# Performance work log

Measured on AMD Instinct MI355X. Metric: run time of the kernel, lower is better.

## Reference

```python
import jax, jax.numpy as jnp
import numpy as np

N, E, F_IN, H, C = 10000, 640000, 128, 128, 40


def setup_inputs() -> dict:
    key = jax.random.key(0)
    ks = jax.random.split(key, 8)
    x = jax.random.normal(ks[0], (N, F_IN), dtype=jnp.float32)
    edge_index = jax.random.randint(ks[1], (2, E), 0, N, dtype=jnp.int64)
    W1 = jax.random.normal(ks[2], (F_IN, H), dtype=jnp.float32) / np.sqrt(F_IN)
    b1 = jnp.zeros((H,), dtype=jnp.float32)
    W2 = jax.random.normal(ks[3], (H, H), dtype=jnp.float32) / np.sqrt(H)
    b2 = jnp.zeros((H,), dtype=jnp.float32)
    Wc = jax.random.normal(ks[4], (H, C), dtype=jnp.float32) / np.sqrt(H)
    bc = jnp.zeros((C,), dtype=jnp.float32)
    return {"x": x, "edge_index": edge_index, "W1": W1, "b1": b1,
            "W2": W2, "b2": b2, "Wc": Wc, "bc": bc}


def _gcn_conv(x, src, dst, norm, W, b):
    # GCNConv: out = D^{-1/2}(A+I)D^{-1/2} (x @ W) + b
    h = x @ W                               # [N, H]
    msg = h[src] * norm[:, None]            # gather + per-edge normalize
    out = jax.ops.segment_sum(msg, dst, num_segments=N)  # scatter-add
    return out + b


def reference(x, edge_index, W1, b1, W2, b2, Wc, bc):
    # add self-loops (as PyG GCNConv does by default)
    loops = jnp.arange(N, dtype=edge_index.dtype)
    src = jnp.concatenate([edge_index[0], loops])   # [E+N]
    dst = jnp.concatenate([edge_index[1], loops])   # [E+N]
    # symmetric normalization deg^{-1/2} with self-loops included
    deg = jax.ops.segment_sum(jnp.ones_like(dst, dtype=x.dtype), dst, num_segments=N)
    dinv = jax.lax.rsqrt(deg)                       # deg >= 1 due to self-loops
    norm = dinv[src] * dinv[dst]                    # [E+N]

    h = _gcn_conv(x, src, dst, norm, W1, b1)
    h = jax.nn.relu(h)
    h = _gcn_conv(h, src, dst, norm, W2, b2)
    logits = h @ Wc + bc                            # [N, C]
    return jax.nn.log_softmax(logits, axis=1)
```

## Files before the change

kernel.cpp:

```cpp
#include <hip/hip_runtime.h>
#include <hip/hip_fp16.h>
#include <math.h>

#define FDIM 128
#define CDIM 40
#define DMAX 192
#define NMAX 10240
#define SLICE_SHIFT 14
#define SLICE_SZ (1 << SLICE_SHIFT)

__device__ __forceinline__ uint2 pack_half4(float4 v) {
    __half2 p0 = __float22half2_rn(make_float2(v.x, v.y));
    __half2 p1 = __float22half2_rn(make_float2(v.z, v.w));
    uint2 u;
    u.x = *(unsigned int*)&p0;
    u.y = *(unsigned int*)&p1;
    return u;
}

__device__ __forceinline__ void unpack_add4(float acc[8], uint4 r) {
    __half2* p = (__half2*)&r;
    #pragma unroll
    for (int q = 0; q < 4; ++q) {
        float2 f = __half22float2(p[q]);
        acc[2 * q]     += f.x;
        acc[2 * q + 1] += f.y;
    }
}

__global__ __launch_bounds__(256) void k_hist(
        const int* __restrict__ dst, unsigned short* __restrict__ lrank,
        int* __restrict__ cnt, int e, int n) {
    __shared__ int h[NMAX];
    int tid = threadIdx.x;
    for (int i = tid; i < n; i += 256) h[i] = 0;
    __syncthreads();
    int base = (int)blockIdx.x << SLICE_SHIFT;
    int end = base + SLICE_SZ; if (end > e) end = e;
    for (int i = base + tid * 4; i < end; i += 1024) {
        if (i + 3 < end) {
            int4 d = *(const int4*)(dst + i);
            int p0 = atomicAdd(&h[d.x], 1);
            int p1 = atomicAdd(&h[d.y], 1);
            int p2 = atomicAdd(&h[d.z], 1);
            int p3 = atomicAdd(&h[d.w], 1);
            ushort4 r;
            r.x = (unsigned short)p0; r.y = (unsigned short)p1;
            r.z = (unsigned short)p2; r.w = (unsigned short)p3;
            *(ushort4*)(lrank + i) = r;
        } else {
            for (int k = i; k < end; ++k)
                lrank[k] = (unsigned short)atomicAdd(&h[dst[k]], 1);
        }
    }
    __syncthreads();
    int* c = cnt + (size_t)blockIdx.x * n;
    for (int i = tid; i < n; i += 256) c[i] = h[i];
}

__global__ __launch_bounds__(256) void k_scan(
        int* __restrict__ cnt, int* __restrict__ deg, int nslice, int n) {
    int v = blockIdx.x * 256 + threadIdx.x;
    if (v >= n) return;
    int s = 0;
    for (int b = 0; b < nslice; ++b) {
        int t = cnt[(size_t)b * n + v];
        cnt[(size_t)b * n + v] = s;
        s += t;
    }
    deg[v] = s;
}

__global__ __launch_bounds__(256) void k_mega(
        const float* __restrict__ A, const float* __restrict__ W,
        const int* __restrict__ deg, uint2* __restrict__ h16, int n,
        const int* __restrict__ src, const int* __restrict__ dst,
        const unsigned short* __restrict__ lrank, const int* __restrict__ base,
        unsigned short* __restrict__ col, int e, int gemm_blocks) {
    __shared__ float As[32][FDIM];
    int tid = threadIdx.x;
    if ((int)blockIdx.x < gemm_blocks) {
        int r0 = blockIdx.x * 32;
        for (int t = tid; t < 32 * 32; t += 256) {
            int r = t >> 5, c4 = t & 31;
            int gr = r0 + r;
            float4 v = make_float4(0.f, 0.f, 0.f, 0.f);
            if (gr < n) v = ((const float4*)A)[(size_t)gr * 32 + c4];
            ((float4*)As[r])[c4] = v;
        }
        __syncthreads();
        int cb = (tid & 31) * 4;
        int rb = (tid >> 5) * 4;
        float4 acc0 = make_float4(0,0,0,0), acc1 = acc0, acc2 = acc0, acc3 = acc0;
        for (int k = 0; k < FDIM; ++k) {
            float4 w = *(const float4*)(W + k * FDIM + cb);
            float a0 = As[rb + 0][k], a1 = As[rb + 1][k];
            float a2 = As[rb + 2][k], a3 = As[rb + 3][k];
            acc0.x += a0 * w.x; acc0.y += a0 * w.y; acc0.z += a0 * w.z; acc0.w += a0 * w.w;
            acc1.x += a1 * w.x; acc1.y += a1 * w.y; acc1.z += a1 * w.z; acc1.w += a1 * w.w;
            acc2.x += a2 * w.x; acc2.y += a2 * w.y; acc2.z += a2 * w.z; acc2.w += a2 * w.w;
            acc3.x += a3 * w.x; acc3.y += a3 * w.y; acc3.z += a3 * w.z; acc3.w += a3 * w.w;
        }
        float4 accs[4] = {acc0, acc1, acc2, acc3};
        #pragma unroll
        for (int i = 0; i < 4; ++i) {
            int gr = r0 + rb + i;
            if (gr < n) {
                float dinv = rsqrtf((float)(deg[gr] + 1));
                float4 v = accs[i];
                v.x *= dinv; v.y *= dinv; v.z *= dinv; v.w *= dinv;
                h16[(size_t)gr * 32 + (cb >> 2)] = pack_half4(v);
            }
        }
    } else {
        int g = ((int)blockIdx.x - gemm_blocks) * 256 + tid;
        int i4 = g * 4;
        if (i4 + 3 < e) {
            const int* bs = base + (size_t)(i4 >> SLICE_SHIFT) * n;
            int4 d = ((const int4*)dst)[g];
            int4 s = ((const int4*)src)[g];
            ushort4 lr = ((const ushort4*)lrank)[g];
            int p0 = bs[d.x] + lr.x;
            int p1 = bs[d.y] + lr.y;
            int p2 = bs[d.z] + lr.z;
            int p3 = bs[d.w] + lr.w;
            if (p0 < DMAX) col[(size_t)d.x * DMAX + p0] = (unsigned short)s.x;
            if (p1 < DMAX) col[(size_t)d.y * DMAX + p1] = (unsigned short)s.y;
            if (p2 < DMAX) col[(size_t)d.z * DMAX + p2] = (unsigned short)s.z;
            if (p3 < DMAX) col[(size_t)d.w * DMAX + p3] = (unsigned short)s.w;
        } else if (i4 < e) {
            for (int k = i4; k < e; ++k) {
                int d = dst[k];
                int p = base[(size_t)(k >> SLICE_SHIFT) * n + d] + lrank[k];
                if (p < DMAX) col[(size_t)d * DMAX + p] = (unsigned short)src[k];
            }
        }
    }
}

template <bool RELU>
__device__ __forceinline__ void agg_gather(
        float out8[8], const uint4* __restrict__ hs,
        const unsigned short* __restrict__ col, const int* __restrict__ deg,
        const float* __restrict__ bias, int node, int l) {
    int dn = deg[node];
    float dinv = rsqrtf((float)(dn + 1));
    if (dn > DMAX) dn = DMAX;
    const uint4* cl8 = (const uint4*)(col + (size_t)node * DMAX);
    float a0[8], a1[8];
    #pragma unroll
    for (int q = 0; q < 8; ++q) { a0[q] = 0.f; a1[q] = 0.f; }
    unpack_add4(a0, hs[(size_t)node * 16 + l]);
    int j = 0;
    for (; j + 16 <= dn; j += 16) {
        uint4 cA = cl8[(j >> 3) + 0];
        uint4 cB = cl8[(j >> 3) + 1];
        int s0 = cA.x & 0xFFFF, s1 = cA.x >> 16;
        int s2 = cA.y & 0xFFFF, s3 = cA.y >> 16;
        int s4 = cA.z & 0xFFFF, s5 = cA.z >> 16;
        int s6 = cA.w & 0xFFFF, s7 = cA.w >> 16;
        int s8 = cB.x & 0xFFFF, s9 = cB.x >> 16;
        int sa = cB.y & 0xFFFF, sb = cB.y >> 16;
        int sc = cB.z & 0xFFFF, sd = cB.z >> 16;
        int se = cB.w & 0xFFFF, sf = cB.w >> 16;
        uint4 q0 = hs[(size_t)s0 * 16 + l];
        uint4 q1 = hs[(size_t)s1 * 16 + l];
        uint4 q2 = hs[(size_t)s2 * 16 + l];
        uint4 q3 = hs[(size_t)s3 * 16 + l];
        uint4 q4 = hs[(size_t)s4 * 16 + l];
        uint4 q5 = hs[(size_t)s5 * 16 + l];
        uint4 q6 = hs[(size_t)s6 * 16 + l];
        uint4 q7 = hs[(size_t)s7 * 16 + l];
        uint4 q8 = hs[(size_t)s8 * 16 + l];
        uint4 q9 = hs[(size_t)s9 * 16 + l];
        uint4 qa = hs[(size_t)sa * 16 + l];
        uint4 qb = hs[(size_t)sb * 16 + l];
        uint4 qc = hs[(size_t)sc * 16 + l];
        uint4 qd = hs[(size_t)sd * 16 + l];
        uint4 qe = hs[(size_t)se * 16 + l];
        uint4 qf = hs[(size_t)sf * 16 + l];
        unpack_add4(a0, q0); unpack_add4(a1, q1);
        unpack_add4(a0, q2); unpack_add4(a1, q3);
        unpack_add4(a0, q4); unpack_add4(a1, q5);
        unpack_add4(a0, q6); unpack_add4(a1, q7);
        unpack_add4(a0, q8); unpack_add4(a1, q9);
        unpack_add4(a0, qa); unpack_add4(a1, qb);
        unpack_add4(a0, qc); unpack_add4(a1, qd);
        unpack_add4(a0, qe); unpack_add4(a1, qf);
    }
    for (; j + 8 <= dn; j += 8) {
        uint4 c = cl8[j >> 3];
        int s0 = c.x & 0xFFFF, s1 = c.x >> 16;
        int s2 = c.y & 0xFFFF, s3 = c.y >> 16;
        int s4 = c.z & 0xFFFF, s5 = c.z >> 16;
        int s6 = c.w & 0xFFFF, s7 = c.w >> 16;
        uint4 q0 = hs[(size_t)s0 * 16 + l];
        uint4 q1 = hs[(size_t)s1 * 16 + l];
        uint4 q2 = hs[(size_t)s2 * 16 + l];
        uint4 q3 = hs[(size_t)s3 * 16 + l];
        uint4 q4 = hs[(size_t)s4 * 16 + l];
        uint4 q5 = hs[(size_t)s5 * 16 + l];
        uint4 q6 = hs[(size_t)s6 * 16 + l];
        uint4 q7 = hs[(size_t)s7 * 16 + l];
        unpack_add4(a0, q0); unpack_add4(a1, q1);
        unpack_add4(a0, q2); unpack_add4(a1, q3);
        unpack_add4(a0, q4); unpack_add4(a1, q5);
        unpack_add4(a0, q6); unpack_add4(a1, q7);
    }
    const unsigned short* cl = col + (size_t)node * DMAX;
    for (; j < dn; ++j) unpack_add4(a0, hs[(size_t)cl[j] * 16 + l]);
    float4 b0 = ((const float4*)bias)[2 * l];
    float4 b1 = ((const float4*)bias)[2 * l + 1];
    float bb[8] = {b0.x, b0.y, b0.z, b0.w, b1.x, b1.y, b1.z, b1.w};
    #pragma unroll
    for (int q = 0; q < 8; ++q) {
        float v = dinv * (a0[q] + a1[q]) + bb[q];
        out8[q] = RELU ? fmaxf(v, 0.f) : v;
    }
}

__global__ __launch_bounds__(128) void k_agg_gemm(
        const uint4* __restrict__ hs1, const unsigned short* __restrict__ col,
        const int* __restrict__ deg, const float* __restrict__ b1,
        const float* __restrict__ W2, uint2* __restrict__ hs2, int n) {
    __shared__ float As[8][FDIM + 4];
    __shared__ float dl[8];
    int tid = threadIdx.x;
    int grp = tid >> 4, l = tid & 15;
    int node = blockIdx.x * 8 + grp;
    if (node < n) {
        float r8[8];
        agg_gather<true>(r8, hs1, col, deg, b1, node, l);
        float4* dst4 = (float4*)&As[grp][8 * l];
        dst4[0] = make_float4(r8[0], r8[1], r8[2], r8[3]);
        dst4[1] = make_float4(r8[4], r8[5], r8[6], r8[7]);
        if (l == 0) dl[grp] = rsqrtf((float)(deg[node] + 1));
    }
    __syncthreads();
    int cb = (tid & 31) * 4;
    int rb = (tid >> 5) * 2;
    float4 acc0 = make_float4(0,0,0,0), acc1 = acc0;
    for (int k = 0; k < FDIM; ++k) {
        float4 w = *(const float4*)(W2 + k * FDIM + cb);
        float x0 = As[rb][k], x1 = As[rb + 1][k];
        acc0.x += x0 * w.x; acc0.y += x0 * w.y; acc0.z += x0 * w.z; acc0.w += x0 * w.w;
        acc1.x += x1 * w.x; acc1.y += x1 * w.y; acc1.z += x1 * w.z; acc1.w += x1 * w.w;
    }
    int g0 = blockIdx.x * 8 + rb;
    if (g0 < n) {
        float s = dl[rb];
        float4 v = acc0;
        v.x *= s; v.y *= s; v.z *= s; v.w *= s;
        hs2[(size_t)g0 * 32 + (cb >> 2)] = pack_half4(v);
    }
    if (g0 + 1 < n) {
        float s = dl[rb + 1];
        float4 v = acc1;
        v.x *= s; v.y *= s; v.z *= s; v.w *= s;
        hs2[(size_t)(g0 + 1) * 32 + (cb >> 2)] = pack_half4(v);
    }
}

__global__ __launch_bounds__(128) void k_agg_cls(
        const uint4* __restrict__ hs2, const unsigned short* __restrict__ col,
        const int* __restrict__ deg, const float* __restrict__ b2,
        const float* __restrict__ Wc, const float* __restrict__ bc,
        float* __restrict__ out, int n) {
    __shared__ float As[8][FDIM + 4];
    int tid = threadIdx.x;
    int grp = tid >> 4, l = tid & 15;
    int node = blockIdx.x * 8 + grp;
    if (node < n) {
        float r8[8];
        agg_gather<false>(r8, hs2, col, deg, b2, node, l);
        float4* dst4 = (float4*)&As[grp][8 * l];
        dst4[0] = make_float4(r8[0], r8[1], r8[2], r8[3]);
        dst4[1] = make_float4(r8[4], r8[5], r8[6], r8[7]);
    }
    __syncthreads();
    int wv = tid >> 6, lane = tid & 63;
    #pragma unroll
    for (int ii = 0; ii < 4; ++ii) {
        int li = wv * 4 + ii;
        int nd = blockIdx.x * 8 + li;
        if (nd >= n) continue;
        const float* row = As[li];
        int c = (lane < CDIM) ? lane : (lane - 24);
        float acc = bc[c];
        for (int k = 0; k < FDIM; k += 4) {
            float a0 = row[k + 0], a1 = row[k + 1];
            float a2 = row[k + 2], a3 = row[k + 3];
            acc += a0 * Wc[(k + 0) * CDIM + c];
            acc += a1 * Wc[(k + 1) * CDIM + c];
            acc += a2 * Wc[(k + 2) * CDIM + c];
            acc += a3 * Wc[(k + 3) * CDIM + c];
        }
        float lv = (lane < CDIM) ? acc : -INFINITY;
        float m = lv;
        for (int off = 32; off > 0; off >>= 1) m = fmaxf(m, __shfl_down(m, off));
        m = __shfl(m, 0);
        float e = (lane < CDIM) ? expf(lv - m) : 0.0f;
        float s = e;
        for (int off = 32; off > 0; off >>= 1) s += __shfl_down(s, off);
        s = __shfl(s, 0);
        if (lane < CDIM) out[(size_t)nd * CDIM + lane] = lv - m - logf(s);
    }
}


extern "C" void kernel_launch(void* const* d_in, const int* in_sizes, int n_in,
                              void* d_out, int out_size, void* d_ws, size_t ws_size,
                              hipStream_t stream) {
    const float* x  = (const float*)d_in[0];
    const int*   ei = (const int*)d_in[1];
    const float* W1 = (const float*)d_in[2];
    const float* b1 = (const float*)d_in[3];
    const float* W2 = (const float*)d_in[4];
    const float* b2 = (const float*)d_in[5];
    const float* Wc = (const float*)d_in[6];
    const float* bc = (const float*)d_in[7];
    float* out = (float*)d_out;

    const int N = in_sizes[0] / FDIM;
    const int E = in_sizes[1] / 2;
    const int* srcp = ei;
    const int* dstp = ei + E;
    const int NSLICE = (E + SLICE_SZ - 1) >> SLICE_SHIFT;

    char* ws = (char*)d_ws;
    auto alloc = [&](size_t bytes) {
        char* p = ws;
        ws += (bytes + 255) & ~(size_t)255;
        return p;
    };
    int*            deg   = (int*)           alloc((size_t)N * 4);
    int*            cnt   = (int*)           alloc((size_t)NSLICE * N * 4);
    unsigned short* lrank = (unsigned short*)alloc((size_t)E * 2);
    unsigned short* col   = (unsigned short*)alloc((size_t)N * DMAX * 2);
    uint4*          h1h   = (uint4*)         alloc((size_t)N * 256);
    uint4*          h2h   = (uint4*)         alloc((size_t)N * 256);

    k_hist<<<NSLICE, 256, 0, stream>>>(dstp, lrank, cnt, E, N);

    k_scan<<<(N + 255) / 256, 256, 0, stream>>>(cnt, deg, NSLICE, N);

    int gb = (N + 31) / 32;
    int fb = (E / 4 + 255) / 256;
    k_mega<<<gb + fb, 256, 0, stream>>>(
        x, W1, deg, (uint2*)h1h, N, srcp, dstp, lrank, cnt, col, E, gb);

    k_agg_gemm<<<(N + 7) / 8, 128, 0, stream>>>(
        h1h, col, deg, b1, W2, (uint2*)h2h, N);

    k_agg_cls<<<(N + 7) / 8, 128, 0, stream>>>(
        h2h, col, deg, b2, Wc, bc, out, N);
}
```

Before: 159.1 us.

## Merge all stages into one cooperative persistent kernel with grid syncs

Replaces the five separate launches (histogram, scan, GEMM+fill, two aggregation stages) with a single cooperative kernel that loops over work units per phase and separates phases with grid-wide syncs. Shared memory is reused across phases through a union, and aggregation units grow to 16 nodes per 256-thread block. This removes inter-kernel launch gaps but caps occupancy to co-resident blocks and adds grid barrier costs, with large shared memory limiting latency hiding in the gather phases.

Measured after the change: 329.8 us. 2.07x slower.

```diff
diff --git a/kernel.cpp b/kernel.cpp
--- a/kernel.cpp
+++ b/kernel.cpp
@@ -1,6 +1,9 @@
 #include <hip/hip_runtime.h>
 #include <hip/hip_fp16.h>
+#include <hip/hip_cooperative_groups.h>
 #include <math.h>
+
+namespace cg = cooperative_groups;
 
 #define FDIM 128
 #define CDIM 40
@@ -25,116 +28,6 @@
         float2 f = __half22float2(p[q]);
         acc[2 * q]     += f.x;
         acc[2 * q + 1] += f.y;
-    }
-}
-
-__global__ __launch_bounds__(256) void k_hist(
-        const int* __restrict__ dst, unsigned short* __restrict__ lrank,
-        int* __restrict__ cnt, int e, int n) {
-    __shared__ int h[NMAX];
-    int tid = threadIdx.x;
-    for (int i = tid; i < n; i += 256) h[i] = 0;
-    __syncthreads();
-    int base = (int)blockIdx.x << SLICE_SHIFT;
-    int end = base + SLICE_SZ; if (end > e) end = e;
-    for (int i = base + tid * 4; i < end; i += 1024) {
-        if (i + 3 < end) {
-            int4 d = *(const int4*)(dst + i);
-            int p0 = atomicAdd(&h[d.x], 1);
-            int p1 = atomicAdd(&h[d.y], 1);
-            int p2 = atomicAdd(&h[d.z], 1);
-            int p3 = atomicAdd(&h[d.w], 1);
-            ushort4 r;
-            r.x = (unsigned short)p0; r.y = (unsigned short)p1;
-            r.z = (unsigned short)p2; r.w = (unsigned short)p3;
-            *(ushort4*)(lrank + i) = r;
-        } else {
-            for (int k = i; k < end; ++k)
-                lrank[k] = (unsigned short)atomicAdd(&h[dst[k]], 1);
-        }
-    }
-    __syncthreads();
-    int* c = cnt + (size_t)blockIdx.x * n;
-    for (int i = tid; i < n; i += 256) c[i] = h[i];
-}
-
-__global__ __launch_bounds__(256) void k_scan(
-        int* __restrict__ cnt, int* __restrict__ deg, int nslice, int n) {
-    int v = blockIdx.x * 256 + threadIdx.x;
-    if (v >= n) return;
-    int s = 0;
-    for (int b = 0; b < nslice; ++b) {
-        int t = cnt[(size_t)b * n + v];
-        cnt[(size_t)b * n + v] = s;
-        s += t;
-    }
-    deg[v] = s;
-}
-
-__global__ __launch_bounds__(256) void k_mega(
-        const float* __restrict__ A, const float* __restrict__ W,
-        const int* __restrict__ deg, uint2* __restrict__ h16, int n,
-        const int* __restrict__ src, const int* __restrict__ dst,
-        const unsigned short* __restrict__ lrank, const int* __restrict__ base,
-        unsigned short* __restrict__ col, int e, int gemm_blocks) {
-    __shared__ float As[32][FDIM];
-    int tid = threadIdx.x;
-    if ((int)blockIdx.x < gemm_blocks) {
-        int r0 = blockIdx.x * 32;
-        for (int t = tid; t < 32 * 32; t += 256) {
-            int r = t >> 5, c4 = t & 31;
-            int gr = r0 + r;
-            float4 v = make_float4(0.f, 0.f, 0.f, 0.f);
-            if (gr < n) v = ((const float4*)A)[(size_t)gr * 32 + c4];
-            ((float4*)As[r])[c4] = v;
-        }
-        __syncthreads();
-        int cb = (tid & 31) * 4;
-        int rb = (tid >> 5) * 4;
-        float4 acc0 = make_float4(0,0,0,0), acc1 = acc0, acc2 = acc0, acc3 = acc0;
-        for (int k = 0; k < FDIM; ++k) {
-            float4 w = *(const float4*)(W + k * FDIM + cb);
-            float a0 = As[rb + 0][k], a1 = As[rb + 1][k];
-            float a2 = As[rb + 2][k], a3 = As[rb + 3][k];
-            acc0.x += a0 * w.x; acc0.y += a0 * w.y; acc0.z += a0 * w.z; acc0.w += a0 * w.w;
-            acc1.x += a1 * w.x; acc1.y += a1 * w.y; acc1.z += a1 * w.z; acc1.w += a1 * w.w;
-            acc2.x += a2 * w.x; acc2.y += a2 * w.y; acc2.z += a2 * w.z; acc2.w += a2 * w.w;
-            acc3.x += a3 * w.x; acc3.y += a3 * w.y; acc3.z += a3 * w.z; acc3.w += a3 * w.w;
-        }
-        float4 accs[4] = {acc0, acc1, acc2, acc3};
-        #pragma unroll
-        for (int i = 0; i < 4; ++i) {
-            int gr = r0 + rb + i;
-            if (gr < n) {
-                float dinv = rsqrtf((float)(deg[gr] + 1));
-                float4 v = accs[i];
-                v.x *= dinv; v.y *= dinv; v.z *= dinv; v.w *= dinv;
-                h16[(size_t)gr * 32 + (cb >> 2)] = pack_half4(v);
-            }
-        }
-    } else {
-        int g = ((int)blockIdx.x - gemm_blocks) * 256 + tid;
-        int i4 = g * 4;
-        if (i4 + 3 < e) {
-            const int* bs = base + (size_t)(i4 >> SLICE_SHIFT) * n;
-            int4 d = ((const int4*)dst)[g];
-            int4 s = ((const int4*)src)[g];
-            ushort4 lr = ((const ushort4*)lrank)[g];
-            int p0 = bs[d.x] + lr.x;
-            int p1 = bs[d.y] + lr.y;
-            int p2 = bs[d.z] + lr.z;
-            int p3 = bs[d.w] + lr.w;
-            if (p0 < DMAX) col[(size_t)d.x * DMAX + p0] = (unsigned short)s.x;
-            if (p1 < DMAX) col[(size_t)d.y * DMAX + p1] = (unsigned short)s.y;
-            if (p2 < DMAX) col[(size_t)d.z * DMAX + p2] = (unsigned short)s.z;
-            if (p3 < DMAX) col[(size_t)d.w * DMAX + p3] = (unsigned short)s.w;
-        } else if (i4 < e) {
-            for (int k = i4; k < e; ++k) {
-                int d = dst[k];
-                int p = base[(size_t)(k >> SLICE_SHIFT) * n + d] + lrank[k];
-                if (p < DMAX) col[(size_t)d * DMAX + p] = (unsigned short)src[k];
-            }
-        }
     }
 }
 
@@ -219,91 +112,211 @@
     }
 }
 
-__global__ __launch_bounds__(128) void k_agg_gemm(
-        const uint4* __restrict__ hs1, const unsigned short* __restrict__ col,
-        const int* __restrict__ deg, const float* __restrict__ b1,
-        const float* __restrict__ W2, uint2* __restrict__ hs2, int n) {
-    __shared__ float As[8][FDIM + 4];
-    __shared__ float dl[8];
+union SharedU {
+    int hist[NMAX];
+    float As32[32][FDIM];
+    struct { float As16[16][FDIM + 4]; float dl[16]; } agg;
+};
+
+__global__ __launch_bounds__(256, 2) void k_all(
+        const float* __restrict__ x, const float* __restrict__ W1,
+        const float* __restrict__ b1, const float* __restrict__ W2,
+        const float* __restrict__ b2, const float* __restrict__ Wc,
+        const float* __restrict__ bc, float* __restrict__ out,
+        int n, int e,
+        const int* __restrict__ src, const int* __restrict__ dst,
+        int* __restrict__ deg, int* __restrict__ cnt,
+        unsigned short* __restrict__ lrank, unsigned short* __restrict__ col,
+        uint4* __restrict__ h1h, uint4* __restrict__ h2h,
+        int nslice, int gb, int fb) {
+    __shared__ SharedU sh;
+    cg::grid_group grid = cg::this_grid();
     int tid = threadIdx.x;
-    int grp = tid >> 4, l = tid & 15;
-    int node = blockIdx.x * 8 + grp;
-    if (node < n) {
-        float r8[8];
-        agg_gather<true>(r8, hs1, col, deg, b1, node, l);
-        float4* dst4 = (float4*)&As[grp][8 * l];
-        dst4[0] = make_float4(r8[0], r8[1], r8[2], r8[3]);
-        dst4[1] = make_float4(r8[4], r8[5], r8[6], r8[7]);
-        if (l == 0) dl[grp] = rsqrtf((float)(deg[node] + 1));
-    }
-    __syncthreads();
-    int cb = (tid & 31) * 4;
-    int rb = (tid >> 5) * 2;
-    float4 acc0 = make_float4(0,0,0,0), acc1 = acc0;
-    for (int k = 0; k < FDIM; ++k) {
-        float4 w = *(const float4*)(W2 + k * FDIM + cb);
-        float x0 = As[rb][k], x1 = As[rb + 1][k];
-        acc0.x += x0 * w.x; acc0.y += x0 * w.y; acc0.z += x0 * w.z; acc0.w += x0 * w.w;
-        acc1.x += x1 * w.x; acc1.y += x1 * w.y; acc1.z += x1 * w.z; acc1.w += x1 * w.w;
-    }
-    int g0 = blockIdx.x * 8 + rb;
-    if (g0 < n) {
-        float s = dl[rb];
-        float4 v = acc0;
-        v.x *= s; v.y *= s; v.z *= s; v.w *= s;
-        hs2[(size_t)g0 * 32 + (cb >> 2)] = pack_half4(v);
-    }
-    if (g0 + 1 < n) {
-        float s = dl[rb + 1];
-        float4 v = acc1;
-        v.x *= s; v.y *= s; v.z *= s; v.w *= s;
-        hs2[(size_t)(g0 + 1) * 32 + (cb >> 2)] = pack_half4(v);
-    }
-}
-
-__global__ __launch_bounds__(128) void k_agg_cls(
-        const uint4* __restrict__ hs2, const unsigned short* __restrict__ col,
-        const int* __restrict__ deg, const float* __restrict__ b2,
-        const float* __restrict__ Wc, const float* __restrict__ bc,
-        float* __restrict__ out, int n) {
-    __shared__ float As[8][FDIM + 4];
-    int tid = threadIdx.x;
-    int grp = tid >> 4, l = tid & 15;
-    int node = blockIdx.x * 8 + grp;
-    if (node < n) {
-        float r8[8];
-        agg_gather<false>(r8, hs2, col, deg, b2, node, l);
-        float4* dst4 = (float4*)&As[grp][8 * l];
-        dst4[0] = make_float4(r8[0], r8[1], r8[2], r8[3]);
-        dst4[1] = make_float4(r8[4], r8[5], r8[6], r8[7]);
-    }
-    __syncthreads();
-    int wv = tid >> 6, lane = tid & 63;
-    #pragma unroll
-    for (int ii = 0; ii < 4; ++ii) {
-        int li = wv * 4 + ii;
-        int nd = blockIdx.x * 8 + li;
-        if (nd >= n) continue;
-        const float* row = As[li];
-        int c = (lane < CDIM) ? lane : (lane - 24);
-        float acc = bc[c];
-        for (int k = 0; k < FDIM; k += 4) {
-            float a0 = row[k + 0], a1 = row[k + 1];
-            float a2 = row[k + 2], a3 = row[k + 3];
-            acc += a0 * Wc[(k + 0) * CDIM + c];
-            acc += a1 * Wc[(k + 1) * CDIM + c];
-            acc += a2 * Wc[(k + 2) * CDIM + c];
-            acc += a3 * Wc[(k + 3) * CDIM + c];
-        }
-        float lv = (lane < CDIM) ? acc : -INFINITY;
-        float m = lv;
-        for (int off = 32; off > 0; off >>= 1) m = fmaxf(m, __shfl_down(m, off));
-        m = __shfl(m, 0);
-        float e = (lane < CDIM) ? expf(lv - m) : 0.0f;
-        float s = e;
-        for (int off = 32; off > 0; off >>= 1) s += __shfl_down(s, off);
-        s = __shfl(s, 0);
-        if (lane < CDIM) out[(size_t)nd * CDIM + lane] = lv - m - logf(s);
+
+    for (int s = blockIdx.x; s < nslice; s += gridDim.x) {
+        for (int i = tid; i < n; i += 256) sh.hist[i] = 0;
+        __syncthreads();
+        int base = s << SLICE_SHIFT;
+        int end = base + SLICE_SZ; if (end > e) end = e;
+        for (int i = base + tid * 4; i < end; i += 1024) {
+            if (i + 3 < end) {
+                int4 d = *(const int4*)(dst + i);
+                int p0 = atomicAdd(&sh.hist[d.x], 1);
+                int p1 = atomicAdd(&sh.hist[d.y], 1);
+                int p2 = atomicAdd(&sh.hist[d.z], 1);
+                int p3 = atomicAdd(&sh.hist[d.w], 1);
+                ushort4 r;
+                r.x = (unsigned short)p0; r.y = (unsigned short)p1;
+                r.z = (unsigned short)p2; r.w = (unsigned short)p3;
+                *(ushort4*)(lrank + i) = r;
+            } else {
+                for (int k = i; k < end; ++k)
+                    lrank[k] = (unsigned short)atomicAdd(&sh.hist[dst[k]], 1);
+            }
+        }
+        __syncthreads();
+        int* c = cnt + (size_t)s * n;
+        for (int i = tid; i < n; i += 256) c[i] = sh.hist[i];
+        __syncthreads();
+    }
+    grid.sync();
+
+    {
+        int stride = (int)gridDim.x * 256;
+        for (int v = (int)blockIdx.x * 256 + tid; v < n; v += stride) {
+            int s = 0;
+            for (int b = 0; b < nslice; ++b) {
+                int t = cnt[(size_t)b * n + v];
+                cnt[(size_t)b * n + v] = s;
+                s += t;
+            }
+            deg[v] = s;
+        }
+    }
+    grid.sync();
+
+    uint2* h16 = (uint2*)h1h;
+    for (int u = blockIdx.x; u < gb + fb; u += gridDim.x) {
+        if (u < gb) {
+            int r0 = u * 32;
+            for (int t = tid; t < 32 * 32; t += 256) {
+                int r = t >> 5, c4 = t & 31;
+                int gr = r0 + r;
+                float4 v = make_float4(0.f, 0.f, 0.f, 0.f);
+                if (gr < n) v = ((const float4*)x)[(size_t)gr * 32 + c4];
+                ((float4*)sh.As32[r])[c4] = v;
+            }
+            __syncthreads();
+            int cb = (tid & 31) * 4;
+            int rb = (tid >> 5) * 4;
+            float4 acc0 = make_float4(0,0,0,0), acc1 = acc0, acc2 = acc0, acc3 = acc0;
+            for (int k = 0; k < FDIM; ++k) {
+                float4 w = *(const float4*)(W1 + k * FDIM + cb);
+                float a0 = sh.As32[rb + 0][k], a1 = sh.As32[rb + 1][k];
+                float a2 = sh.As32[rb + 2][k], a3 = sh.As32[rb + 3][k];
+                acc0.x += a0 * w.x; acc0.y += a0 * w.y; acc0.z += a0 * w.z; acc0.w += a0 * w.w;
+                acc1.x += a1 * w.x; acc1.y += a1 * w.y; acc1.z += a1 * w.z; acc1.w += a1 * w.w;
+                acc2.x += a2 * w.x; acc2.y += a2 * w.y; acc2.z += a2 * w.z; acc2.w += a2 * w.w;
+                acc3.x += a3 * w.x; acc3.y += a3 * w.y; acc3.z += a3 * w.z; acc3.w += a3 * w.w;
+            }
+            float4 accs[4] = {acc0, acc1, acc2, acc3};
+            #pragma unroll
+            for (int i = 0; i < 4; ++i) {
+                int gr = r0 + rb + i;
+                if (gr < n) {
+                    float dinv = rsqrtf((float)(deg[gr] + 1));
+                    float4 v = accs[i];
+                    v.x *= dinv; v.y *= dinv; v.z *= dinv; v.w *= dinv;
+                    h16[(size_t)gr * 32 + (cb >> 2)] = pack_half4(v);
+                }
+            }
+            __syncthreads();
+        } else {
+            int g = (u - gb) * 256 + tid;
+            int i4 = g * 4;
+            if (i4 + 3 < e) {
+                const int* bs = cnt + (size_t)(i4 >> SLICE_SHIFT) * n;
+                int4 d = ((const int4*)dst)[g];
+                int4 s = ((const int4*)src)[g];
+                ushort4 lr = ((const ushort4*)lrank)[g];
+                int p0 = bs[d.x] + lr.x;
+                int p1 = bs[d.y] + lr.y;
+                int p2 = bs[d.z] + lr.z;
+                int p3 = bs[d.w] + lr.w;
+                if (p0 < DMAX) col[(size_t)d.x * DMAX + p0] = (unsigned short)s.x;
+                if (p1 < DMAX) col[(size_t)d.y * DMAX + p1] = (unsigned short)s.y;
+                if (p2 < DMAX) col[(size_t)d.z * DMAX + p2] = (unsigned short)s.z;
+                if (p3 < DMAX) col[(size_t)d.w * DMAX + p3] = (unsigned short)s.w;
+            } else if (i4 < e) {
+                for (int k = i4; k < e; ++k) {
+                    int d = dst[k];
+                    int p = cnt[(size_t)(k >> SLICE_SHIFT) * n + d] + lrank[k];
+                    if (p < DMAX) col[(size_t)d * DMAX + p] = (unsigned short)src[k];
+                }
+            }
+        }
+    }
+    grid.sync();
+
+    uint2* hs2w = (uint2*)h2h;
+    int dunits = (n + 15) / 16;
+    for (int u = blockIdx.x; u < dunits; u += gridDim.x) {
+        int grp = tid >> 4, l = tid & 15;
+        int node = u * 16 + grp;
+        if (node < n) {
+            float r8[8];
+            agg_gather<true>(r8, h1h, col, deg, b1, node, l);
+            float4* d4 = (float4*)&sh.agg.As16[grp][8 * l];
+            d4[0] = make_float4(r8[0], r8[1], r8[2], r8[3]);
+            d4[1] = make_float4(r8[4], r8[5], r8[6], r8[7]);
+            if (l == 0) sh.agg.dl[grp] = rsqrtf((float)(deg[node] + 1));
+        }
+        __syncthreads();
+        int cb = (tid & 31) * 4;
+        int rb = (tid >> 5) * 2;
+        float4 acc0 = make_float4(0,0,0,0), acc1 = acc0;
+        for (int k = 0; k < FDIM; ++k) {
+            float4 w = *(const float4*)(W2 + k * FDIM + cb);
+            float x0 = sh.agg.As16[rb][k], x1 = sh.agg.As16[rb + 1][k];
+            acc0.x += x0 * w.x; acc0.y += x0 * w.y; acc0.z += x0 * w.z; acc0.w += x0 * w.w;
+            acc1.x += x1 * w.x; acc1.y += x1 * w.y; acc1.z += x1 * w.z; acc1.w += x1 * w.w;
+        }
+        int g0 = u * 16 + rb;
+        if (g0 < n) {
+            float s = sh.agg.dl[rb];
+            float4 v = acc0;
+            v.x *= s; v.y *= s; v.z *= s; v.w *= s;
+            hs2w[(size_t)g0 * 32 + (cb >> 2)] = pack_half4(v);
+        }
+        if (g0 + 1 < n) {
+            float s = sh.agg.dl[rb + 1];
+            float4 v = acc1;
+            v.x *= s; v.y *= s; v.z *= s; v.w *= s;
+            hs2w[(size_t)(g0 + 1) * 32 + (cb >> 2)] = pack_half4(v);
+        }
+        __syncthreads();
+    }
+    grid.sync();
+
+    for (int u = blockIdx.x; u < dunits; u += gridDim.x) {
+        int grp = tid >> 4, l = tid & 15;
+        int node = u * 16 + grp;
+        if (node < n) {
+            float r8[8];
+            agg_gather<false>(r8, h2h, col, deg, b2, node, l);
+            float4* d4 = (float4*)&sh.agg.As16[grp][8 * l];
+            d4[0] = make_float4(r8[0], r8[1], r8[2], r8[3]);
+            d4[1] = make_float4(r8[4], r8[5], r8[6], r8[7]);
+        }
+        __syncthreads();
+        int wv = tid >> 6, lane = tid & 63;
+        #pragma unroll
+        for (int ii = 0; ii < 4; ++ii) {
+            int li = wv * 4 + ii;
+            int nd = u * 16 + li;
+            if (nd >= n) continue;
+            const float* row = sh.agg.As16[li];
+            int c = (lane < CDIM) ? lane : (lane - 24);
+            float acc = bc[c];
+            for (int k = 0; k < FDIM; k += 4) {
+                float a0 = row[k + 0], a1 = row[k + 1];
+                float a2 = row[k + 2], a3 = row[k + 3];
+                acc += a0 * Wc[(k + 0) * CDIM + c];
+                acc += a1 * Wc[(k + 1) * CDIM + c];
+                acc += a2 * Wc[(k + 2) * CDIM + c];
+                acc += a3 * Wc[(k + 3) * CDIM + c];
+            }
+            float lv = (lane < CDIM) ? acc : -INFINITY;
+            float m = lv;
+            for (int off = 32; off > 0; off >>= 1) m = fmaxf(m, __shfl_down(m, off));
+            m = __shfl(m, 0);
+            float e2 = (lane < CDIM) ? expf(lv - m) : 0.0f;
+            float s = e2;
+            for (int off = 32; off > 0; off >>= 1) s += __shfl_down(s, off);
+            s = __shfl(s, 0);
+            if (lane < CDIM) out[(size_t)nd * CDIM + lane] = lv - m - logf(s);
+        }
+        __syncthreads();
     }
 }
 
@@ -321,11 +334,11 @@
     const float* bc = (const float*)d_in[7];
     float* out = (float*)d_out;
 
-    const int N = in_sizes[0] / FDIM;
-    const int E = in_sizes[1] / 2;
+    int N = in_sizes[0] / FDIM;
+    int E = in_sizes[1] / 2;
     const int* srcp = ei;
     const int* dstp = ei + E;
-    const int NSLICE = (E + SLICE_SZ - 1) >> SLICE_SHIFT;
+    int NSLICE = (E + SLICE_SZ - 1) >> SLICE_SHIFT;
 
     char* ws = (char*)d_ws;
     auto alloc = [&](size_t bytes) {
@@ -340,18 +353,23 @@
     uint4*          h1h   = (uint4*)         alloc((size_t)N * 256);
     uint4*          h2h   = (uint4*)         alloc((size_t)N * 256);
 
-    k_hist<<<NSLICE, 256, 0, stream>>>(dstp, lrank, cnt, E, N);
-
-    k_scan<<<(N + 255) / 256, 256, 0, stream>>>(cnt, deg, NSLICE, N);
-
     int gb = (N + 31) / 32;
     int fb = (E / 4 + 255) / 256;
-    k_mega<<<gb + fb, 256, 0, stream>>>(
-        x, W1, deg, (uint2*)h1h, N, srcp, dstp, lrank, cnt, col, E, gb);
-
-    k_agg_gemm<<<(N + 7) / 8, 128, 0, stream>>>(
-        h1h, col, deg, b1, W2, (uint2*)h2h, N);
-
-    k_agg_cls<<<(N + 7) / 8, 128, 0, stream>>>(
-        h2h, col, deg, b2, Wc, bc, out, N);
-}
+
+    int occ = 0;
+    hipError_t oerr = hipOccupancyMaxActiveBlocksPerMultiprocessor(
+        &occ, (const void*)k_all, 256, 0);
+    int G = (oerr == hipSuccess && occ > 0) ? occ * 256 : 512;
+    int maxUnits = gb + fb;
+    if (G > maxUnits) G = maxUnits;
+
+    void* args[] = {
+        (void*)&x, (void*)&W1, (void*)&b1, (void*)&W2, (void*)&b2,
+        (void*)&Wc, (void*)&bc, (void*)&out, (void*)&N, (void*)&E,
+        (void*)&srcp, (void*)&dstp, (void*)&deg, (void*)&cnt,
+        (void*)&lrank, (void*)&col, (void*)&h1h, (void*)&h2h,
+        (void*)&NSLICE, (void*)&gb, (void*)&fb
+    };
+    hipLaunchCooperativeKernel((const void*)k_all, dim3(G), dim3(256),
+                               args, 0, stream);
+}
```
